# Kernel tuning notes

Measured on AMD Instinct MI355X. Metric: run time of the kernel, lower is better.

## Reference

```python
import jax, jax.numpy as jnp
import numpy as np

B, S, D, H = 2, 2048, 256, 8


def setup_inputs() -> dict:
    key = jax.random.key(0)
    ks = jax.random.split(key, 9)
    s = 1.0 / np.sqrt(D)
    x = jax.random.normal(ks[0], (B, S, D), dtype=jnp.float32)
    Wq = jax.random.normal(ks[1], (H, D, D), dtype=jnp.float32) * s
    Wk = jax.random.normal(ks[2], (H, D, D), dtype=jnp.float32) * s
    Wv = jax.random.normal(ks[3], (H, D, D), dtype=jnp.float32) * s
    bq = jnp.zeros((H, D), dtype=jnp.float32)
    bk = jnp.zeros((H, D), dtype=jnp.float32)
    bv = jnp.zeros((H, D), dtype=jnp.float32)
    Wo = jax.random.normal(ks[4], (H * D, D), dtype=jnp.float32) * (1.0 / np.sqrt(H * D))
    bo = jnp.zeros((D,), dtype=jnp.float32)
    return {"x": x, "Wq": Wq, "bq": bq, "Wk": Wk, "bk": bk, "Wv": Wv, "bv": bv, "Wo": Wo, "bo": bo}


def reference(x, Wq, bq, Wk, bk, Wv, bv, Wo, bo):
    # Per-head Q/K/V projections, batched over heads via einsum.
    # q,k,v: [B, H, S, D]
    q = jnp.einsum('bsd,hde->bhse', x, Wq) + bq[None, :, None, :]
    k = jnp.einsum('bsd,hde->bhse', x, Wk) + bk[None, :, None, :]
    v = jnp.einsum('bsd,hde->bhse', x, Wv) + bv[None, :, None, :]
    scale = 1.0 / jnp.sqrt(jnp.asarray(D, dtype=x.dtype))
    scores = jnp.einsum('bhse,bhte->bhst', q, k) * scale  # [B,H,S,S]
    attn = jax.nn.softmax(scores, axis=-1)
    o = jnp.einsum('bhst,bhte->bhse', attn, v)  # [B,H,S,D]
    # Concat heads along feature dim: [B,S,H*D]
    concat = o.transpose(0, 2, 1, 3).reshape(B, S, H * D)
    return concat @ Wo + bo
```

## Files before the change

kernel.cpp:

```cpp
#include <hip/hip_runtime.h>

typedef __bf16 bf16x8 __attribute__((ext_vector_type(8)));
typedef __bf16 bf16x4 __attribute__((ext_vector_type(4)));
typedef float  f32x4  __attribute__((ext_vector_type(4)));
typedef float  f32x16 __attribute__((ext_vector_type(16)));

#define DEVI __device__ __forceinline__

DEVI bf16x8 ld8(const __bf16* p) { return *reinterpret_cast<const bf16x8*>(p); }
DEVI f32x4 mfma16(bf16x8 a, bf16x8 b, f32x4 c) {
  return __builtin_amdgcn_mfma_f32_16x16x32_bf16(a, b, c, 0, 0, 0);
}
DEVI f32x16 mfma32(bf16x8 a, bf16x8 b, f32x16 c) {
  return __builtin_amdgcn_mfma_f32_32x32x16_bf16(a, b, c, 0, 0, 0);
}
DEVI void gl_lds16(const void* g, void* l) {
  __builtin_amdgcn_global_load_lds((__attribute__((address_space(1))) void*)g,
                                   (__attribute__((address_space(3))) void*)l, 16, 0, 0);
}
DEVI unsigned pk2(float a, float b) {
  union { __bf16 h[2]; unsigned u; } x;
  x.h[0] = (__bf16)a; x.h[1] = (__bf16)b; return x.u;
}

#if __has_builtin(__builtin_amdgcn_exp2f)
#define EXP2(x) __builtin_amdgcn_exp2f(x)
#else
#define EXP2(x) exp2f(x)
#endif

__global__ __launch_bounds__(256) void k_prep(
    const float* __restrict__ x, const float* __restrict__ Wq,
    const float* __restrict__ Wk, const float* __restrict__ Wv,
    const float* __restrict__ Wo, __bf16* __restrict__ xb,
    __bf16* __restrict__ Wt, __bf16* __restrict__ Woh, __bf16* __restrict__ Wol) {
  const int bid = blockIdx.x;
  if (bid < 1024) {
    const int i = bid * 256 + threadIdx.x;
    f32x4 v = reinterpret_cast<const f32x4*>(x)[i];
    bf16x4 o;
    o[0] = (__bf16)v[0]; o[1] = (__bf16)v[1]; o[2] = (__bf16)v[2]; o[3] = (__bf16)v[3];
    reinterpret_cast<bf16x4*>(xb)[i] = o;
    return;
  }
  __shared__ float t[32][33];
  const int flat = bid - 1024;
  const float* in; __bf16* oh; __bf16* ol = nullptr;
  int R, C, c0, r0;
  bool lo = false;
  if (flat < 1536) {
    const int which = flat >> 9, rem = flat & 511;
    const int h = rem >> 6, tt = rem & 63;
    c0 = (tt & 7) * 32; r0 = (tt >> 3) * 32;
    const float* Wsrc = which == 0 ? Wq : which == 1 ? Wk : Wv;
    in = Wsrc + h * 65536;
    oh = Wt + which * 524288 + h * 65536;
    R = 256; C = 256;
  } else {
    const int rem = flat - 1536;
    c0 = (rem & 7) * 32; r0 = (rem >> 3) * 32;
    in = Wo; oh = Woh; ol = Wol; lo = true;
    R = 2048; C = 256;
  }
  const int tx = threadIdx.x & 31, ty = threadIdx.x >> 5;
  #pragma unroll
  for (int k = 0; k < 32; k += 8)
    t[ty + k][tx] = in[(size_t)(r0 + ty + k) * C + c0 + tx];
  __syncthreads();
  #pragma unroll
  for (int k = 0; k < 32; k += 8) {
    const float v = t[tx][ty + k];
    const size_t o = (size_t)(c0 + ty + k) * R + r0 + tx;
    const __bf16 h = (__bf16)v;
    oh[o] = h;
    if (lo) ol[o] = (__bf16)(v - (float)h);
  }
}

__global__ __launch_bounds__(256) void k_qkv(
    const __bf16* __restrict__ xb, const __bf16* __restrict__ Wt,
    const float* __restrict__ bq, const float* __restrict__ bk, const float* __restrict__ bv,
    __bf16* __restrict__ Qb, __bf16* __restrict__ Kb, __bf16* __restrict__ Vtb) {
  const int wl = threadIdx.x >> 6, lane = threadIdx.x & 63;
  const int g = lane >> 4, qc = lane & 15;
  const int h = blockIdx.z >> 1, isV = blockIdx.z & 1;
  const int sblk = blockIdx.x * 256;
  const int s0 = sblk + wl * 64;
  const int e0 = blockIdx.y * 64;
  const int b = sblk >> 11;
  const int bh = b * 8 + h;
  const int sm0 = s0 & 2047;

  if (isV) {
    const __bf16* Wm = Wt + 2 * 524288 + (size_t)h * 65536;
    const float* bias = bv + h * 256;
    f32x4 acc[4][4] = {};
    #pragma unroll
    for (int kk = 0; kk < 8; kk++) {
      bf16x8 af[4], bf[4];
      #pragma unroll
      for (int ai = 0; ai < 4; ai++)
        af[ai] = ld8(xb + (size_t)(s0 + ai * 16 + qc) * 256 + kk * 32 + g * 8);
      #pragma unroll
      for (int bj = 0; bj < 4; bj++)
        bf[bj] = ld8(Wm + (size_t)(e0 + bj * 16 + qc) * 256 + kk * 32 + g * 8);
      #pragma unroll
      for (int ai = 0; ai < 4; ai++)
        #pragma unroll
        for (int bj = 0; bj < 4; bj++)
          acc[ai][bj] = mfma16(af[ai], bf[bj], acc[ai][bj]);
    }
    #pragma unroll
    for (int bj = 0; bj < 4; bj++) {
      const int e = e0 + bj * 16 + qc;
      const float be = bias[e];
      #pragma unroll
      for (int ai = 0; ai < 4; ai++) {
        bf16x4 pk;
        #pragma unroll
        for (int r = 0; r < 4; r++) pk[r] = (__bf16)(acc[ai][bj][r] + be);
        *reinterpret_cast<bf16x4*>(Vtb + ((size_t)(bh * 256 + e)) * 2048 +
                                   sm0 + ai * 16 + g * 4) = pk;
      }
    }
  } else {
    const __bf16* WmQ = Wt + (size_t)h * 65536;
    const __bf16* WmK = Wt + 524288 + (size_t)h * 65536;
    f32x4 accq[4][4] = {}, acck[4][4] = {};
    #pragma unroll
    for (int kk = 0; kk < 8; kk++) {
      bf16x8 aq[4], ak[4], bf[4];
      #pragma unroll
      for (int ai = 0; ai < 4; ai++) {
        aq[ai] = ld8(WmQ + (size_t)(e0 + ai * 16 + qc) * 256 + kk * 32 + g * 8);
        ak[ai] = ld8(WmK + (size_t)(e0 + ai * 16 + qc) * 256 + kk * 32 + g * 8);
      }
      #pragma unroll
      for (int bj = 0; bj < 4; bj++)
        bf[bj] = ld8(xb + (size_t)(s0 + bj * 16 + qc) * 256 + kk * 32 + g * 8);
      #pragma unroll
      for (int ai = 0; ai < 4; ai++)
        #pragma unroll
        for (int bj = 0; bj < 4; bj++) {
          accq[ai][bj] = mfma16(aq[ai], bf[bj], accq[ai][bj]);
          acck[ai][bj] = mfma16(ak[ai], bf[bj], acck[ai][bj]);
        }
    }
    const float sc = 0.0625f * 1.4426950408889634f;
    #pragma unroll
    for (int ai = 0; ai < 4; ai++) {
      float beq[4], bek[4];
      #pragma unroll
      for (int r = 0; r < 4; r++) {
        beq[r] = bq[h * 256 + e0 + ai * 16 + g * 4 + r];
        bek[r] = bk[h * 256 + e0 + ai * 16 + g * 4 + r];
      }
      #pragma unroll
      for (int bj = 0; bj < 4; bj++) {
        const int srow = sm0 + bj * 16 + qc;
        const size_t base = ((size_t)(bh * 2048 + srow)) * 256 + e0 + ai * 16 + g * 4;
        bf16x4 pq, pk;
        #pragma unroll
        for (int r = 0; r < 4; r++) {
          pq[r] = (__bf16)((accq[ai][bj][r] + beq[r]) * sc);
          pk[r] = (__bf16)(acck[ai][bj][r] + bek[r]);
        }
        *reinterpret_cast<bf16x4*>(Qb + base) = pq;
        *reinterpret_cast<bf16x4*>(Kb + base) = pk;
      }
    }
  }
}

__global__ __launch_bounds__(256) void k_attn(
    const __bf16* __restrict__ Qb, const __bf16* __restrict__ Kb,
    const __bf16* __restrict__ Vtb, __bf16* __restrict__ Oh, __bf16* __restrict__ Ol) {
  __shared__ __align__(16) unsigned char smem[131072];
  const int tid = threadIdx.x;
  const int wl = tid >> 6, lane = tid & 63;
  const int hi = lane >> 5, q = lane & 31;

  const int bid = blockIdx.x;
  const int s = (bid & 7) * 32 + (bid >> 3);
  const int bh = s >> 4, qt = s & 15;

  const int q0w = qt * 128 + wl * 32;
  const char* Kg = (const char*)Kb + ((size_t)bh * 2048) * 512;
  const char* Vg = (const char*)Vtb + (size_t)bh * 256 * 4096;
  const __bf16* Qp = Qb + ((size_t)(bh * 2048 + q0w + q)) * 256;

  bf16x8 qf[16];
  #pragma unroll
  for (int kk = 0; kk < 16; kk++) qf[kk] = ld8(Qp + kk * 16 + hi * 8);

  f32x16 acc[8];
  #pragma unroll
  for (int i = 0; i < 8; i++)
    #pragma unroll
    for (int e = 0; e < 16; e++) acc[i][e] = 0.f;

  auto stage = [&](int nb, int t) {
    unsigned char* kbp = smem + nb * 32768 + wl * 8192;
    unsigned char* vbp = smem + 65536 + nb * 32768 + wl * 8192;
    #pragma unroll
    for (int j = 0; j < 8; j++) {
      const int O = wl * 8192 + j * 1024 + lane * 16;
      const int kv = O >> 9;
      const int c = ((O >> 4) & 31) ^ (kv & 15);
      gl_lds16(Kg + (size_t)t * 32768 + (size_t)kv * 512 + c * 16, kbp + j * 1024);
    }
    #pragma unroll
    for (int j = 0; j < 8; j++) {
      const int O = wl * 8192 + j * 1024 + lane * 16;
      const int sb = O >> 10;
      const int kvh = (O >> 9) & 1;
      const int dlo = (O >> 6) & 7;
      const int ci = (O >> 4) & 3;
      const int d = sb * 8 + dlo;
      gl_lds16(Vg + (size_t)d * 4096 + (size_t)t * 128 + kvh * 64 + ((ci ^ (sb & 3)) << 4),
               vbp + j * 1024);
    }
  };

  float m_run = -3.0e38f, l_run = 0.f;
  stage(0, 0);
  __syncthreads();

  for (int t = 0; t < 32; t++) {
    const int cur = t & 1;
    const unsigned char* kbc = smem + cur * 32768;
    const unsigned char* vbc = smem + 65536 + cur * 32768;
    if (t < 31) stage(cur ^ 1, t + 1);

    f32x16 st0, st1;
    #pragma unroll
    for (int e = 0; e < 16; e++) { st0[e] = 0.f; st1[e] = 0.f; }
    #pragma unroll
    for (int kk = 0; kk < 16; kk++) {
      const int o0 = q * 512 + ((((kk << 1) + hi) ^ (q & 15)) << 4);
      bf16x8 k0 = *reinterpret_cast<const bf16x8*>(kbc + o0);
      bf16x8 k1 = *reinterpret_cast<const bf16x8*>(kbc + o0 + 16384);
      st0 = mfma32(k0, qf[kk], st0);
      st1 = mfma32(k1, qf[kk], st1);
    }

    f32x16 mx;
    #pragma unroll
    for (int r = 0; r < 16; r++) mx[r] = fmaxf(st0[r], st1[r]);
    #pragma unroll
    for (int w2 = 8; w2 > 0; w2 >>= 1)
      #pragma unroll
      for (int r = 0; r < w2; r++) mx[r] = fmaxf(mx[r], mx[r + w2]);
    const float rmax = fmaxf(mx[0], __shfl_xor(mx[0], 32));
    if (__any(rmax > m_run + 8.0f)) {
      const float m_new = fmaxf(rmax, m_run);
      const float alpha = EXP2(m_run - m_new);
      m_run = m_new;
      l_run *= alpha;
      #pragma unroll
      for (int r = 0; r < 16; r++) {
        const float ar = __shfl(alpha, (r & 3) + 8 * (r >> 2) + 4 * hi);
        #pragma unroll
        for (int dt = 0; dt < 8; dt++) acc[dt][r] *= ar;
      }
    }
    f32x16 sm_;
    #pragma unroll
    for (int r = 0; r < 16; r++) {
      st0[r] = EXP2(st0[r] - m_run);
      st1[r] = EXP2(st1[r] - m_run);
      sm_[r] = st0[r] + st1[r];
    }
    #pragma unroll
    for (int w2 = 8; w2 > 0; w2 >>= 1)
      #pragma unroll
      for (int r = 0; r < w2; r++) sm_[r] += sm_[r + w2];
    l_run += sm_[0] + __shfl_xor(sm_[0], 32);

    bf16x8 pa[4];
    #define MKCHUNK(STV, H2, OUT) {                          \
      const unsigned L0 = pk2(STV[H2 * 8 + 0], STV[H2 * 8 + 1]);  \
      const unsigned L1 = pk2(STV[H2 * 8 + 2], STV[H2 * 8 + 3]);  \
      const unsigned H0 = pk2(STV[H2 * 8 + 4], STV[H2 * 8 + 5]);  \
      const unsigned H1 = pk2(STV[H2 * 8 + 6], STV[H2 * 8 + 7]);  \
      const unsigned xL0 = __shfl_xor(L0, 32), xL1 = __shfl_xor(L1, 32); \
      const unsigned xH0 = __shfl_xor(H0, 32), xH1 = __shfl_xor(H1, 32); \
      unsigned pw[4];                                        \
      pw[0] = hi ? xH0 : L0;  pw[1] = hi ? xH1 : L1;         \
      pw[2] = hi ? H0 : xL0;  pw[3] = hi ? H1 : xL1;         \
      OUT = *reinterpret_cast<bf16x8*>(pw); }
    MKCHUNK(st0, 0, pa[0]); MKCHUNK(st0, 1, pa[1]);
    MKCHUNK(st1, 0, pa[2]); MKCHUNK(st1, 1, pa[3]);
    #undef MKCHUNK

    #pragma unroll
    for (int dt = 0; dt < 8; dt++) {
      const int d = dt * 32 + q;
      const int base = (d >> 3) * 1024 + (d & 7) * 64;
      const int key = (d >> 3) & 3;
      #pragma unroll
      for (int c = 0; c < 4; c++) {
        const int off = base + (c >> 1) * 512 +
                        (((((c & 1) << 1) | hi) ^ key) << 4);
        bf16x8 vf = *reinterpret_cast<const bf16x8*>(vbc + off);
        acc[dt] = mfma32(pa[c], vf, acc[dt]);
      }
    }
    __syncthreads();
  }

  float linv[16];
  #pragma unroll
  for (int r = 0; r < 16; r++)
    linv[r] = 1.f / __shfl(l_run, (r & 3) + 8 * (r >> 2) + 4 * hi);
  const int b = bh >> 3, h = bh & 7;
  #pragma unroll
  for (int dt = 0; dt < 8; dt++) {
    #pragma unroll
    for (int r = 0; r < 16; r++) {
      const float v = acc[dt][r] * linv[r];
      const int qrow = (r & 3) + 8 * (r >> 2) + 4 * hi;
      const size_t off = (size_t)b * (2048 * 2048) +
                         (size_t)(q0w + qrow) * 2048 + h * 256 + dt * 32 + q;
      const __bf16 hv = (__bf16)v;
      Oh[off] = hv;
      Ol[off] = (__bf16)(v - (float)hv);
    }
  }
}

__global__ __launch_bounds__(256) void k_out(
    const __bf16* __restrict__ Oh, const __bf16* __restrict__ Ol,
    const __bf16* __restrict__ Wh, const __bf16* __restrict__ Wl,
    const float* __restrict__ bo, float* __restrict__ out) {
  const int w = threadIdx.x >> 6, lane = threadIdx.x & 63;
  const int g = lane >> 4, qc = lane & 15;
  const int m0 = blockIdx.x * 64 + w * 16, n0 = blockIdx.y * 64;
  const int k0 = blockIdx.z * 512;
  f32x4 acc[4] = {};
  const __bf16* ah_p = Oh + (size_t)(m0 + qc) * 2048 + k0 + g * 8;
  const __bf16* al_p = Ol + (size_t)(m0 + qc) * 2048 + k0 + g * 8;
  for (int kk = 0; kk < 16; kk++) {
    bf16x8 ah = ld8(ah_p + kk * 32);
    bf16x8 al = ld8(al_p + kk * 32);
    #pragma unroll
    for (int nt = 0; nt < 4; nt++) {
      const size_t nrow = (size_t)(n0 + nt * 16 + qc) * 2048 + k0 + kk * 32 + g * 8;
      bf16x8 bh = ld8(Wh + nrow);
      bf16x8 bl = ld8(Wl + nrow);
      acc[nt] = mfma16(ah, bh, acc[nt]);
      acc[nt] = mfma16(al, bh, acc[nt]);
      acc[nt] = mfma16(ah, bl, acc[nt]);
    }
  }
  #pragma unroll
  for (int nt = 0; nt < 4; nt++) {
    const int n = n0 + nt * 16 + qc;
    const float bb = (blockIdx.z == 0) ? bo[n] : 0.f;
    #pragma unroll
    for (int r = 0; r < 4; r++)
      unsafeAtomicAdd(&out[(m0 + g * 4 + r) * 256 + n], acc[nt][r] + bb);
  }
}

extern "C" void kernel_launch(void* const* d_in, const int* in_sizes, int n_in,
                              void* d_out, int out_size, void* d_ws, size_t ws_size,
                              hipStream_t stream) {
  const float* x  = (const float*)d_in[0];
  const float* Wq = (const float*)d_in[1];
  const float* bq = (const float*)d_in[2];
  const float* Wk = (const float*)d_in[3];
  const float* bk = (const float*)d_in[4];
  const float* Wv = (const float*)d_in[5];
  const float* bv = (const float*)d_in[6];
  const float* Wo = (const float*)d_in[7];
  const float* bo = (const float*)d_in[8];
  char* p = (char*)d_ws;
  __bf16* xb  = (__bf16*)(p);
  __bf16* Wt  = (__bf16*)(p + (2ull  << 20));
  __bf16* Woh = (__bf16*)(p + (5ull  << 20));
  __bf16* Wol = (__bf16*)(p + (6ull  << 20));
  __bf16* Qb  = (__bf16*)(p + (7ull  << 20));
  __bf16* Kb  = (__bf16*)(p + (23ull << 20));
  __bf16* Vtb = (__bf16*)(p + (39ull << 20));
  __bf16* Ohb = (__bf16*)(p + (55ull << 20));
  __bf16* Olb = (__bf16*)(p + (71ull << 20));

  k_prep<<<dim3(3072), dim3(256), 0, stream>>>(x, Wq, Wk, Wv, Wo, xb, Wt, Woh, Wol);
  k_qkv<<<dim3(16, 4, 16), dim3(256), 0, stream>>>(xb, Wt, bq, bk, bv, Qb, Kb, Vtb);
  k_attn<<<dim3(256), dim3(256), 0, stream>>>(Qb, Kb, Vtb, Ohb, Olb);
  (void)hipMemsetAsync(d_out, 0, (size_t)out_size * sizeof(float), stream);
  k_out<<<dim3(64, 4, 4), dim3(256), 0, stream>>>(Ohb, Olb, Woh, Wol, bo, (float*)d_out);
}
```

Baseline: 251.4 us.

## Split attention blocks across head-dim halves and halve KV tile

The attention kernel now launches 512 blocks instead of 256. Each block handles 64 query rows, and its four waves are split as two query subtiles by two halves of the value head dimension. The KV tile shrinks from 64 to 32 keys per iteration, which halves shared memory to 64KB and halves the accumulator registers per wave. The goal is better occupancy and load balance across the CUs. The cost is that QK^T scores are computed twice, once by each head-dim half wave pair, the loop runs twice as many iterations with more barriers, and K is loaded redundantly.

```diff
diff --git a/kernel.cpp b/kernel.cpp
--- a/kernel.cpp
+++ b/kernel.cpp
@@ -175,16 +175,17 @@
 __global__ __launch_bounds__(256) void k_attn(
     const __bf16* __restrict__ Qb, const __bf16* __restrict__ Kb,
     const __bf16* __restrict__ Vtb, __bf16* __restrict__ Oh, __bf16* __restrict__ Ol) {
-  __shared__ __align__(16) unsigned char smem[131072];
+  __shared__ __align__(16) unsigned char smem[65536];
   const int tid = threadIdx.x;
   const int wl = tid >> 6, lane = tid & 63;
   const int hi = lane >> 5, q = lane & 31;
+  const int qs = wl & 1, dh = wl >> 1;
 
   const int bid = blockIdx.x;
-  const int s = (bid & 7) * 32 + (bid >> 3);
-  const int bh = s >> 4, qt = s & 15;
-
-  const int q0w = qt * 128 + wl * 32;
+  const int s = (bid & 7) * 64 + (bid >> 3);
+  const int bh = s >> 5, qt = s & 31;
+
+  const int q0w = qt * 64 + qs * 32;
   const char* Kg = (const char*)Kb + ((size_t)bh * 2048) * 512;
   const char* Vg = (const char*)Vtb + (size_t)bh * 256 * 4096;
   const __bf16* Qp = Qb + ((size_t)(bh * 2048 + q0w + q)) * 256;
@@ -193,31 +194,30 @@
   #pragma unroll
   for (int kk = 0; kk < 16; kk++) qf[kk] = ld8(Qp + kk * 16 + hi * 8);
 
-  f32x16 acc[8];
-  #pragma unroll
-  for (int i = 0; i < 8; i++)
+  f32x16 acc[4];
+  #pragma unroll
+  for (int i = 0; i < 4; i++)
     #pragma unroll
     for (int e = 0; e < 16; e++) acc[i][e] = 0.f;
 
   auto stage = [&](int nb, int t) {
-    unsigned char* kbp = smem + nb * 32768 + wl * 8192;
-    unsigned char* vbp = smem + 65536 + nb * 32768 + wl * 8192;
-    #pragma unroll
-    for (int j = 0; j < 8; j++) {
-      const int O = wl * 8192 + j * 1024 + lane * 16;
+    unsigned char* kbp = smem + nb * 16384 + wl * 4096;
+    unsigned char* vbp = smem + 32768 + nb * 16384 + wl * 4096;
+    #pragma unroll
+    for (int j = 0; j < 4; j++) {
+      const int O = wl * 4096 + j * 1024 + lane * 16;
       const int kv = O >> 9;
       const int c = ((O >> 4) & 31) ^ (kv & 15);
-      gl_lds16(Kg + (size_t)t * 32768 + (size_t)kv * 512 + c * 16, kbp + j * 1024);
-    }
-    #pragma unroll
-    for (int j = 0; j < 8; j++) {
-      const int O = wl * 8192 + j * 1024 + lane * 16;
-      const int sb = O >> 10;
-      const int kvh = (O >> 9) & 1;
+      gl_lds16(Kg + (size_t)t * 16384 + (size_t)kv * 512 + c * 16, kbp + j * 1024);
+    }
+    #pragma unroll
+    for (int j = 0; j < 4; j++) {
+      const int O = wl * 4096 + j * 1024 + lane * 16;
+      const int sb = O >> 9;
       const int dlo = (O >> 6) & 7;
-      const int ci = (O >> 4) & 3;
+      const int ch = (O >> 4) & 3;
       const int d = sb * 8 + dlo;
-      gl_lds16(Vg + (size_t)d * 4096 + (size_t)t * 128 + kvh * 64 + ((ci ^ (sb & 3)) << 4),
+      gl_lds16(Vg + (size_t)d * 4096 + (size_t)t * 64 + ((ch ^ (sb & 3)) << 4),
                vbp + j * 1024);
     }
   };
@@ -226,27 +226,23 @@
   stage(0, 0);
   __syncthreads();
 
-  for (int t = 0; t < 32; t++) {
+  for (int t = 0; t < 64; t++) {
     const int cur = t & 1;
-    const unsigned char* kbc = smem + cur * 32768;
-    const unsigned char* vbc = smem + 65536 + cur * 32768;
-    if (t < 31) stage(cur ^ 1, t + 1);
-
-    f32x16 st0, st1;
-    #pragma unroll
-    for (int e = 0; e < 16; e++) { st0[e] = 0.f; st1[e] = 0.f; }
+    const unsigned char* kbc = smem + cur * 16384;
+    const unsigned char* vbc = smem + 32768 + cur * 16384;
+    if (t < 63) stage(cur ^ 1, t + 1);
+
+    f32x16 st;
+    #pragma unroll
+    for (int e = 0; e < 16; e++) st[e] = 0.f;
     #pragma unroll
     for (int kk = 0; kk < 16; kk++) {
       const int o0 = q * 512 + ((((kk << 1) + hi) ^ (q & 15)) << 4);
-      bf16x8 k0 = *reinterpret_cast<const bf16x8*>(kbc + o0);
-      bf16x8 k1 = *reinterpret_cast<const bf16x8*>(kbc + o0 + 16384);
-      st0 = mfma32(k0, qf[kk], st0);
-      st1 = mfma32(k1, qf[kk], st1);
-    }
-
-    f32x16 mx;
-    #pragma unroll
-    for (int r = 0; r < 16; r++) mx[r] = fmaxf(st0[r], st1[r]);
+      bf16x8 kf = *reinterpret_cast<const bf16x8*>(kbc + o0);
+      st = mfma32(kf, qf[kk], st);
+    }
+
+    f32x16 mx = st;
     #pragma unroll
     for (int w2 = 8; w2 > 0; w2 >>= 1)
       #pragma unroll
@@ -261,15 +257,14 @@
       for (int r = 0; r < 16; r++) {
         const float ar = __shfl(alpha, (r & 3) + 8 * (r >> 2) + 4 * hi);
         #pragma unroll
-        for (int dt = 0; dt < 8; dt++) acc[dt][r] *= ar;
+        for (int dt = 0; dt < 4; dt++) acc[dt][r] *= ar;
       }
     }
     f32x16 sm_;
     #pragma unroll
     for (int r = 0; r < 16; r++) {
-      st0[r] = EXP2(st0[r] - m_run);
-      st1[r] = EXP2(st1[r] - m_run);
-      sm_[r] = st0[r] + st1[r];
+      st[r] = EXP2(st[r] - m_run);
+      sm_[r] = st[r];
     }
     #pragma unroll
     for (int w2 = 8; w2 > 0; w2 >>= 1)
@@ -277,31 +272,30 @@
       for (int r = 0; r < w2; r++) sm_[r] += sm_[r + w2];
     l_run += sm_[0] + __shfl_xor(sm_[0], 32);
 
-    bf16x8 pa[4];
-    #define MKCHUNK(STV, H2, OUT) {                          \
-      const unsigned L0 = pk2(STV[H2 * 8 + 0], STV[H2 * 8 + 1]);  \
-      const unsigned L1 = pk2(STV[H2 * 8 + 2], STV[H2 * 8 + 3]);  \
-      const unsigned H0 = pk2(STV[H2 * 8 + 4], STV[H2 * 8 + 5]);  \
-      const unsigned H1 = pk2(STV[H2 * 8 + 6], STV[H2 * 8 + 7]);  \
-      const unsigned xL0 = __shfl_xor(L0, 32), xL1 = __shfl_xor(L1, 32); \
-      const unsigned xH0 = __shfl_xor(H0, 32), xH1 = __shfl_xor(H1, 32); \
-      unsigned pw[4];                                        \
-      pw[0] = hi ? xH0 : L0;  pw[1] = hi ? xH1 : L1;         \
-      pw[2] = hi ? H0 : xL0;  pw[3] = hi ? H1 : xL1;         \
-      OUT = *reinterpret_cast<bf16x8*>(pw); }
-    MKCHUNK(st0, 0, pa[0]); MKCHUNK(st0, 1, pa[1]);
-    MKCHUNK(st1, 0, pa[2]); MKCHUNK(st1, 1, pa[3]);
-    #undef MKCHUNK
-
-    #pragma unroll
-    for (int dt = 0; dt < 8; dt++) {
-      const int d = dt * 32 + q;
-      const int base = (d >> 3) * 1024 + (d & 7) * 64;
-      const int key = (d >> 3) & 3;
-      #pragma unroll
-      for (int c = 0; c < 4; c++) {
-        const int off = base + (c >> 1) * 512 +
-                        (((((c & 1) << 1) | hi) ^ key) << 4);
+    bf16x8 pa[2];
+    #pragma unroll
+    for (int c = 0; c < 2; c++) {
+      const unsigned L0 = pk2(st[c * 8 + 0], st[c * 8 + 1]);
+      const unsigned L1 = pk2(st[c * 8 + 2], st[c * 8 + 3]);
+      const unsigned H0 = pk2(st[c * 8 + 4], st[c * 8 + 5]);
+      const unsigned H1 = pk2(st[c * 8 + 6], st[c * 8 + 7]);
+      const unsigned xL0 = __shfl_xor(L0, 32), xL1 = __shfl_xor(L1, 32);
+      const unsigned xH0 = __shfl_xor(H0, 32), xH1 = __shfl_xor(H1, 32);
+      unsigned pw[4];
+      pw[0] = hi ? xH0 : L0;  pw[1] = hi ? xH1 : L1;
+      pw[2] = hi ? H0 : xL0;  pw[3] = hi ? H1 : xL1;
+      pa[c] = *reinterpret_cast<bf16x8*>(pw);
+    }
+
+    #pragma unroll
+    for (int dt = 0; dt < 4; dt++) {
+      const int d = dh * 128 + dt * 32 + q;
+      const int sb = d >> 3;
+      const int base = sb * 512 + (d & 7) * 64;
+      const int key = sb & 3;
+      #pragma unroll
+      for (int c = 0; c < 2; c++) {
+        const int off = base + ((((c << 1) | hi) ^ key) << 4);
         bf16x8 vf = *reinterpret_cast<const bf16x8*>(vbc + off);
         acc[dt] = mfma32(pa[c], vf, acc[dt]);
       }
@@ -315,13 +309,13 @@
     linv[r] = 1.f / __shfl(l_run, (r & 3) + 8 * (r >> 2) + 4 * hi);
   const int b = bh >> 3, h = bh & 7;
   #pragma unroll
-  for (int dt = 0; dt < 8; dt++) {
+  for (int dt = 0; dt < 4; dt++) {
     #pragma unroll
     for (int r = 0; r < 16; r++) {
       const float v = acc[dt][r] * linv[r];
       const int qrow = (r & 3) + 8 * (r >> 2) + 4 * hi;
       const size_t off = (size_t)b * (2048 * 2048) +
-                         (size_t)(q0w + qrow) * 2048 + h * 256 + dt * 32 + q;
+                         (size_t)(q0w + qrow) * 2048 + h * 256 + dh * 128 + dt * 32 + q;
       const __bf16 hv = (__bf16)v;
       Oh[off] = hv;
       Ol[off] = (__bf16)(v - (float)hv);
@@ -388,7 +382,7 @@
 
   k_prep<<<dim3(3072), dim3(256), 0, stream>>>(x, Wq, Wk, Wv, Wo, xb, Wt, Woh, Wol);
   k_qkv<<<dim3(16, 4, 16), dim3(256), 0, stream>>>(xb, Wt, bq, bk, bv, Qb, Kb, Vtb);
-  k_attn<<<dim3(256), dim3(256), 0, stream>>>(Qb, Kb, Vtb, Ohb, Olb);
+  k_attn<<<dim3(512), dim3(256), 0, stream>>>(Qb, Kb, Vtb, Ohb, Olb);
   (void)hipMemsetAsync(d_out, 0, (size_t)out_size * sizeof(float), stream);
   k_out<<<dim3(64, 4, 4), dim3(256), 0, stream>>>(Ohb, Olb, Woh, Wol, bo, (float*)d_out);
 }
```

Measured after the change: 302.0 us. +20.1%, slower.
